# Optimization experiments

Measured on AMD Instinct MI355X. Metric: run time of the kernel, lower is better.

## Reference

```python
import jax, jax.numpy as jnp
import numpy as np

EMB = 512
HEADS = 8


def setup_inputs() -> dict:
    key = jax.random.key(0)
    ks = jax.random.split(key, 6)
    b, t, e, h = 4, 1024, EMB, HEADS
    s = 1.0 / np.sqrt(e)
    x = jax.random.normal(ks[0], (b, t, e), dtype=jnp.float32)
    Wq = jax.random.uniform(ks[1], (e, h * e), dtype=jnp.float32, minval=-s, maxval=s)
    Wk = jax.random.uniform(ks[2], (e, h * e), dtype=jnp.float32, minval=-s, maxval=s)
    Wv = jax.random.uniform(ks[3], (e, h * e), dtype=jnp.float32, minval=-s, maxval=s)
    su = 1.0 / np.sqrt(h * e)
    Wu = jax.random.uniform(ks[4], (h * e, e), dtype=jnp.float32, minval=-su, maxval=su)
    bu = jax.random.uniform(ks[5], (e,), dtype=jnp.float32, minval=-su, maxval=su)
    return {"x": x, "Wq": Wq, "Wk": Wk, "Wv": Wv, "Wu": Wu, "bu": bu}


def reference(x, Wq, Wk, Wv, Wu, bu):
    b, t, e = x.shape
    h = HEADS
    # projections: each head gets a FULL e-dim subspace -> [b, t, h, e]
    q = (x @ Wq).reshape(b, t, h, e)
    k = (x @ Wk).reshape(b, t, h, e)
    v = (x @ Wv).reshape(b, t, h, e)
    # scores [b, h, tq, tk], scaled by sqrt(e)
    scores = jnp.einsum("bqhe,bkhe->bhqk", q, k) / jnp.sqrt(jnp.float32(e))
    # causal mask: strictly upper triangle -> -inf (diagonal kept)
    causal = jnp.tril(jnp.ones((t, t), dtype=bool))
    scores = jnp.where(causal[None, None], scores, jnp.float32(-jnp.inf))
    attn = jax.nn.softmax(scores, axis=-1)
    out = jnp.einsum("bhqk,bkhe->bqhe", attn, v).reshape(b, t, h * e)
    return out @ Wu + bu
```

## Files before the change

### kernel.cpp

```cpp
#include <hip/hip_runtime.h>

typedef __attribute__((ext_vector_type(8))) short s16x8;
typedef __attribute__((ext_vector_type(4))) float f32x4;
typedef unsigned short u16;
typedef unsigned int u32;

#define MFMA(A, B, C) __builtin_amdgcn_mfma_f32_16x16x32_bf16(A, B, C, 0, 0, 0)

__device__ __forceinline__ u16 f2bf(float f) {
  u32 u = __builtin_bit_cast(u32, f);
  u += 0x7fffu + ((u >> 16) & 1u);
  return (u16)(u >> 16);
}

__device__ __forceinline__ void gl2lds16(const void* g, void* l) {
  __builtin_amdgcn_global_load_lds(
      (const __attribute__((address_space(1))) void*)g,
      (__attribute__((address_space(3))) void*)l, 16, 0, 0);
}


__global__ __launch_bounds__(256) void cvt_f32_bf16(const float* __restrict__ in,
                                                    u16* __restrict__ out, int n8) {
  int i = blockIdx.x * 256 + threadIdx.x;
  if (i >= n8) return;
  const float4* p = (const float4*)in + (size_t)i * 2;
  float4 a = p[0], b = p[1];
  union { u16 h[8]; uint4 v; } u;
  u.h[0] = f2bf(a.x); u.h[1] = f2bf(a.y); u.h[2] = f2bf(a.z); u.h[3] = f2bf(a.w);
  u.h[4] = f2bf(b.x); u.h[5] = f2bf(b.y); u.h[6] = f2bf(b.z); u.h[7] = f2bf(b.w);
  ((uint4*)out)[i] = u.v;
}

__global__ __launch_bounds__(256) void transpose_cvt(const float* __restrict__ in,
                                                     u16* __restrict__ out, int R, int C) {
  __shared__ float tile[32][33];
  int c0 = blockIdx.x * 32, r0 = blockIdx.y * 32;
  int tx = threadIdx.x, ty = threadIdx.y;
  #pragma unroll
  for (int i = ty; i < 32; i += 8)
    tile[i][tx] = in[(size_t)(r0 + i) * C + c0 + tx];
  __syncthreads();
  #pragma unroll
  for (int i = ty; i < 32; i += 8)
    out[(size_t)(c0 + i) * R + r0 + tx] = f2bf(tile[tx][i]);
}

template <int BF16_OUT>
__global__ __launch_bounds__(256, 2) void gemm_bt(
    const u16* __restrict__ A, const u16* __restrict__ Bt,
    u16* __restrict__ Cb, float* __restrict__ Cf, const float* __restrict__ bias,
    int M, int N, int K) {
  __shared__ u16 alds[128][64];
  __shared__ u16 blds[128][64];
  const int tid = threadIdx.x;
  const int lane = tid & 63, wid = tid >> 6;
  const int wm = (wid >> 1) * 64, wn = (wid & 1) * 64;
  const int m0 = blockIdx.y * 128, n0 = blockIdx.x * 128;

  const int srow = lane >> 3;
  const int scol = (lane & 7) * 8;

  f32x4 acc[4][4];
  #pragma unroll
  for (int m = 0; m < 4; m++)
    #pragma unroll
    for (int n = 0; n < 4; n++) acc[m][n] = {0.f, 0.f, 0.f, 0.f};

  for (int k0 = 0; k0 < K; k0 += 64) {
    __syncthreads();
    #pragma unroll
    for (int i = 0; i < 4; i++) {
      int rbase = (wid * 4 + i) * 8;
      int grow = rbase + srow;
      gl2lds16(&A [(size_t)(m0 + grow) * K + k0 + scol], &alds[rbase][0]);
      gl2lds16(&Bt[(size_t)(n0 + grow) * K + k0 + scol], &blds[rbase][0]);
    }
    __syncthreads();
    #pragma unroll
    for (int kk = 0; kk < 2; kk++) {
      s16x8 af[4], bf[4];
      #pragma unroll
      for (int m = 0; m < 4; m++)
        af[m] = *(const s16x8*)&alds[wm + m * 16 + (lane & 15)][kk * 32 + (lane >> 4) * 8];
      #pragma unroll
      for (int n = 0; n < 4; n++)
        bf[n] = *(const s16x8*)&blds[wn + n * 16 + (lane & 15)][kk * 32 + (lane >> 4) * 8];
      #pragma unroll
      for (int m = 0; m < 4; m++)
        #pragma unroll
        for (int n = 0; n < 4; n++)
          acc[m][n] = MFMA(af[m], bf[n], acc[m][n]);
    }
  }

  #pragma unroll
  for (int m = 0; m < 4; m++)
    #pragma unroll
    for (int n = 0; n < 4; n++) {
      int col = n0 + wn + n * 16 + (lane & 15);
      #pragma unroll
      for (int r = 0; r < 4; r++) {
        int row = m0 + wm + m * 16 + (lane >> 4) * 4 + r;
        float v = acc[m][n][r];
        if (BF16_OUT) Cb[(size_t)row * N + col] = f2bf(v);
        else          Cf[(size_t)row * N + col] = v + bias[col];
      }
    }
}

__global__ __launch_bounds__(256, 2) void attn_fwd(
    const u16* __restrict__ Qg, const u16* __restrict__ Kg, const u16* __restrict__ VTg,
    u16* __restrict__ AO) {
  __shared__ u16 klds[32][512];
  __shared__ u16 vt[512][32];
  __shared__ u16 plds[4][16][40];

  const int tid = threadIdx.x, lane = tid & 63, w = tid >> 6;
  const int l15 = lane & 15, l16 = lane >> 4;

  int idx = blockIdx.x;
  int half = idx >> 8, rr_ = idx & 255;
  const int bh = rr_ & 31;
  int qb = rr_ >> 5;
  if (half) qb = 15 - qb;
  const int b = bh >> 3, h = bh & 7;

  const size_t RS = 4096;
  const u16* Qb  = Qg  + ((size_t)b * 1024) * RS + h * 512;
  const u16* Kb  = Kg  + ((size_t)b * 1024) * RS + h * 512;
  const u16* VTb = VTg + ((size_t)h * 512) * RS + b * 1024;

  const int qrow = qb * 64 + w * 16 + l15;
  s16x8 aq[16];
  #pragma unroll
  for (int kc = 0; kc < 16; kc++)
    aq[kc] = *(const s16x8*)&Qb[(size_t)qrow * RS + kc * 32 + l16 * 8];

  f32x4 acc[32];
  #pragma unroll
  for (int n = 0; n < 32; n++) acc[n] = {0.f, 0.f, 0.f, 0.f};
  float m = -1e30f, lsum = 0.f;

  const int nsteps = 2 * qb + 2;
  const float scale = 0.044194173824159216f;

  for (int s = 0; s < nsteps; s++) {
    __syncthreads();
    #pragma unroll
    for (int i = 0; i < 8; i++) {
      int R = w * 8 + i;
      gl2lds16(&Kb[(size_t)(s * 32 + R) * RS + (size_t)((lane ^ (R & 7)) * 8)],
               &klds[R][0]);
    }
    #pragma unroll
    for (int i = 0; i < 8; i++) {
      int vr0 = (w * 8 + i) * 16;
      gl2lds16(&VTb[(size_t)(vr0 + (lane >> 2)) * RS + s * 32
                    + (size_t)(((lane & 3) ^ ((lane >> 3) & 3)) * 8)],
               &vt[vr0][0]);
    }
    __syncthreads();

    f32x4 s0 = {0.f, 0.f, 0.f, 0.f}, s1 = {0.f, 0.f, 0.f, 0.f};
    #pragma unroll
    for (int kc = 0; kc < 16; kc++) {
      int ch = ((kc * 4 + l16) ^ (l15 & 7)) * 8;
      s16x8 bk0 = *(const s16x8*)&klds[l15][ch];
      s16x8 bk1 = *(const s16x8*)&klds[16 + l15][ch];
      s0 = MFMA(bk0, aq[kc], s0);
      s1 = MFMA(bk1, aq[kc], s1);
    }

    float p[8];
    float pmax = -1e30f;
    #pragma unroll
    for (int r = 0; r < 4; r++) {
      int kv0 = s * 32 + l16 * 4 + r;
      float v0 = (kv0      <= qrow) ? s0[r] * scale : -1e30f;
      float v1 = (kv0 + 16 <= qrow) ? s1[r] * scale : -1e30f;
      p[r] = v0; p[4 + r] = v1;
      pmax = fmaxf(pmax, fmaxf(v0, v1));
    }
    pmax = fmaxf(pmax, __shfl_xor(pmax, 16));
    pmax = fmaxf(pmax, __shfl_xor(pmax, 32));

    int need = __any(pmax > m + 8.f);
    float sf = 1.f;
    if (need) {
      float mnew = fmaxf(m, pmax);
      sf = __expf(m - mnew);
      m = mnew;
    }
    float psum = 0.f;
    #pragma unroll
    for (int j = 0; j < 8; j++) { p[j] = __expf(p[j] - m); psum += p[j]; }
    psum += __shfl_xor(psum, 16);
    psum += __shfl_xor(psum, 32);
    lsum = lsum * sf + psum;

    if (need) {
      float sfr[4];
      #pragma unroll
      for (int r = 0; r < 4; r++) sfr[r] = __shfl(sf, l16 * 4 + r);
      #pragma unroll
      for (int n = 0; n < 32; n++)
        #pragma unroll
        for (int r = 0; r < 4; r++) acc[n][r] *= sfr[r];
    }

    #pragma unroll
    for (int r = 0; r < 4; r++) {
      plds[w][l15][l16 * 4 + r]      = f2bf(p[r]);
      plds[w][l15][16 + l16 * 4 + r] = f2bf(p[4 + r]);
    }
    s16x8 pa = *(const s16x8*)&plds[w][l15][l16 * 8];
    #pragma unroll
    for (int n = 0; n < 32; n++) {
      s16x8 bv = *(const s16x8*)&vt[n * 16 + l15][(l16 ^ ((l15 >> 1) & 3)) * 8];
      acc[n] = MFMA(pa, bv, acc[n]);
    }
  }

  float linv[4];
  #pragma unroll
  for (int r = 0; r < 4; r++) linv[r] = 1.f / __shfl(lsum, l16 * 4 + r);
  #pragma unroll
  for (int n = 0; n < 32; n++)
    #pragma unroll
    for (int r = 0; r < 4; r++) {
      int trow = b * 1024 + qb * 64 + w * 16 + l16 * 4 + r;
      AO[(size_t)trow * RS + h * 512 + n * 16 + l15] = f2bf(acc[n][r] * linv[r]);
    }
}

extern "C" void kernel_launch(void* const* d_in, const int* in_sizes, int n_in,
                              void* d_out, int out_size, void* d_ws, size_t ws_size,
                              hipStream_t stream) {
  const float* x  = (const float*)d_in[0];
  const float* Wq = (const float*)d_in[1];
  const float* Wk = (const float*)d_in[2];
  const float* Wv = (const float*)d_in[3];
  const float* Wu = (const float*)d_in[4];
  const float* bu = (const float*)d_in[5];
  float* out = (float*)d_out;

  const size_t T = 4096;
  const size_t E = 512;
  const size_t HE = 4096;

  char* ws = (char*)d_ws;
  u16* xb  = (u16*)ws; ws += T * E * 2;
  u16* WqT = (u16*)ws; ws += HE * E * 2;
  u16* WkT = (u16*)ws; ws += HE * E * 2;
  u16* WvT = (u16*)ws; ws += HE * E * 2;
  u16* WuT = (u16*)ws; ws += E * HE * 2;
  u16* Qm  = (u16*)ws; ws += T * HE * 2;
  u16* Km  = (u16*)ws; ws += T * HE * 2;
  u16* VTm = (u16*)ws; ws += T * HE * 2;
  u16* AO  = Qm;

  cvt_f32_bf16<<<dim3((T * E / 8 + 255) / 256), dim3(256), 0, stream>>>(x, xb, (int)(T * E / 8));
  {
    dim3 blk(32, 8);
    transpose_cvt<<<dim3(HE / 32, E / 32), blk, 0, stream>>>(Wq, WqT, (int)E, (int)HE);
    transpose_cvt<<<dim3(HE / 32, E / 32), blk, 0, stream>>>(Wk, WkT, (int)E, (int)HE);
    transpose_cvt<<<dim3(HE / 32, E / 32), blk, 0, stream>>>(Wv, WvT, (int)E, (int)HE);
    transpose_cvt<<<dim3(E / 32, HE / 32), blk, 0, stream>>>(Wu, WuT, (int)HE, (int)E);
  }

  {
    dim3 grid(HE / 128, T / 128), blk(256);
    gemm_bt<1><<<grid, blk, 0, stream>>>(xb, WqT, Qm, nullptr, nullptr, (int)T, (int)HE, (int)E);
    gemm_bt<1><<<grid, blk, 0, stream>>>(xb, WkT, Km, nullptr, nullptr, (int)T, (int)HE, (int)E);
  }
  {
    dim3 grid(T / 128, HE / 128), blk(256);
    gemm_bt<1><<<grid, blk, 0, stream>>>(WvT, xb, VTm, nullptr, nullptr, (int)HE, (int)T, (int)E);
  }

  attn_fwd<<<dim3(512), dim3(256), 0, stream>>>(Qm, Km, VTm, AO);

  {
    dim3 grid(E / 128, T / 128), blk(256);
    gemm_bt<0><<<grid, blk, 0, stream>>>(AO, WuT, nullptr, out, bu, (int)T, (int)E, (int)HE);
  }
}
```

Measured before the change: 403.3 us.

## Double-buffer K/V tiles in attention kernel with prefetch and MFMA priority

The attention kernel now double-buffers its K and V^T shared-memory tiles. It issues the global-to-LDS load for the next step before computing the current one, and needs only one barrier per step instead of two. It also wraps the MFMA loops in s_setprio, packs the P stores into 64-bit writes, and orders blocks longest-first (qb descending) instead of pairing halves. The doubled LDS footprint drops occupancy to one block per CU (launch_bounds 256,1), so it trades latency hiding across blocks for hiding within a block.

```diff
diff --git a/kernel.cpp b/kernel.cpp
--- a/kernel.cpp
+++ b/kernel.cpp
@@ -4,6 +4,7 @@
 typedef __attribute__((ext_vector_type(4))) float f32x4;
 typedef unsigned short u16;
 typedef unsigned int u32;
+typedef unsigned long long u64;
 
 #define MFMA(A, B, C) __builtin_amdgcn_mfma_f32_16x16x32_bf16(A, B, C, 0, 0, 0)
 
@@ -109,21 +110,18 @@
     }
 }
 
-__global__ __launch_bounds__(256, 2) void attn_fwd(
+__global__ __launch_bounds__(256, 1) void attn_fwd(
     const u16* __restrict__ Qg, const u16* __restrict__ Kg, const u16* __restrict__ VTg,
     u16* __restrict__ AO) {
-  __shared__ u16 klds[32][512];
-  __shared__ u16 vt[512][32];
+  __shared__ u16 klds[2][32][512];
+  __shared__ u16 vt[2][512][32];
   __shared__ u16 plds[4][16][40];
 
   const int tid = threadIdx.x, lane = tid & 63, w = tid >> 6;
   const int l15 = lane & 15, l16 = lane >> 4;
 
-  int idx = blockIdx.x;
-  int half = idx >> 8, rr_ = idx & 255;
-  const int bh = rr_ & 31;
-  int qb = rr_ >> 5;
-  if (half) qb = 15 - qb;
+  const int qb = 15 - (blockIdx.x >> 5);
+  const int bh = blockIdx.x & 31;
   const int b = bh >> 3, h = bh & 7;
 
   const size_t RS = 4096;
@@ -137,40 +135,48 @@
   for (int kc = 0; kc < 16; kc++)
     aq[kc] = *(const s16x8*)&Qb[(size_t)qrow * RS + kc * 32 + l16 * 8];
 
-  f32x4 acc[32];
-  #pragma unroll
-  for (int n = 0; n < 32; n++) acc[n] = {0.f, 0.f, 0.f, 0.f};
-  float m = -1e30f, lsum = 0.f;
-
   const int nsteps = 2 * qb + 2;
   const float scale = 0.044194173824159216f;
 
-  for (int s = 0; s < nsteps; s++) {
-    __syncthreads();
+  auto STAGE = [&](int s, int buf) {
     #pragma unroll
     for (int i = 0; i < 8; i++) {
       int R = w * 8 + i;
       gl2lds16(&Kb[(size_t)(s * 32 + R) * RS + (size_t)((lane ^ (R & 7)) * 8)],
-               &klds[R][0]);
+               &klds[buf][R][0]);
     }
     #pragma unroll
     for (int i = 0; i < 8; i++) {
       int vr0 = (w * 8 + i) * 16;
       gl2lds16(&VTb[(size_t)(vr0 + (lane >> 2)) * RS + s * 32
                     + (size_t)(((lane & 3) ^ ((lane >> 3) & 3)) * 8)],
-               &vt[vr0][0]);
-    }
-    __syncthreads();
+               &vt[buf][vr0][0]);
+    }
+  };
+
+  f32x4 acc[32];
+  #pragma unroll
+  for (int n = 0; n < 32; n++) acc[n] = {0.f, 0.f, 0.f, 0.f};
+  float m = -1e30f, lsum = 0.f;
+
+  STAGE(0, 0);
+  __syncthreads();
+  int cur = 0;
+
+  for (int s = 0; s < nsteps; s++) {
+    if (s + 1 < nsteps) STAGE(s + 1, cur ^ 1);
 
     f32x4 s0 = {0.f, 0.f, 0.f, 0.f}, s1 = {0.f, 0.f, 0.f, 0.f};
+    __builtin_amdgcn_s_setprio(1);
     #pragma unroll
     for (int kc = 0; kc < 16; kc++) {
       int ch = ((kc * 4 + l16) ^ (l15 & 7)) * 8;
-      s16x8 bk0 = *(const s16x8*)&klds[l15][ch];
-      s16x8 bk1 = *(const s16x8*)&klds[16 + l15][ch];
+      s16x8 bk0 = *(const s16x8*)&klds[cur][l15][ch];
+      s16x8 bk1 = *(const s16x8*)&klds[cur][16 + l15][ch];
       s0 = MFMA(bk0, aq[kc], s0);
       s1 = MFMA(bk1, aq[kc], s1);
     }
+    __builtin_amdgcn_s_setprio(0);
 
     float p[8];
     float pmax = -1e30f;
@@ -209,17 +215,24 @@
         for (int r = 0; r < 4; r++) acc[n][r] *= sfr[r];
     }
 
-    #pragma unroll
-    for (int r = 0; r < 4; r++) {
-      plds[w][l15][l16 * 4 + r]      = f2bf(p[r]);
-      plds[w][l15][16 + l16 * 4 + r] = f2bf(p[4 + r]);
+    {
+      union { u16 h[4]; u64 q; } w0, w1;
+      #pragma unroll
+      for (int r = 0; r < 4; r++) { w0.h[r] = f2bf(p[r]); w1.h[r] = f2bf(p[4 + r]); }
+      *(u64*)&plds[w][l15][l16 * 4]      = w0.q;
+      *(u64*)&plds[w][l15][16 + l16 * 4] = w1.q;
     }
     s16x8 pa = *(const s16x8*)&plds[w][l15][l16 * 8];
+    __builtin_amdgcn_s_setprio(1);
     #pragma unroll
     for (int n = 0; n < 32; n++) {
-      s16x8 bv = *(const s16x8*)&vt[n * 16 + l15][(l16 ^ ((l15 >> 1) & 3)) * 8];
+      s16x8 bv = *(const s16x8*)&vt[cur][n * 16 + l15][(l16 ^ ((l15 >> 1) & 3)) * 8];
       acc[n] = MFMA(pa, bv, acc[n]);
     }
+    __builtin_amdgcn_s_setprio(0);
+
+    __syncthreads();
+    cur ^= 1;
   }
 
   float linv[4];
```

New measurement: 366.2 us. 1.1x faster.
